# Performance work log

Measured on AMD Instinct MI355X. Metric: run time of the kernel, lower is better.

The kernel has to match this reference:

```python
import jax, jax.numpy as jnp
import numpy as np
from jax import lax

B, C, H, W, G = 16, 256, 96, 96, 16


def setup_inputs() -> dict:
    key = jax.random.key(0)
    ks = jax.random.split(key, 8)
    return {
        "x": jax.random.normal(ks[0], (B, C, H, W), jnp.float32),
        "in_w": jax.random.normal(ks[1], (C, C), jnp.float32) / np.sqrt(C).astype(np.float32),
        "gn1_w": jnp.ones((C,), jnp.float32),
        "gn1_b": jnp.zeros((C,), jnp.float32),
        "a_p": jnp.zeros((4, C), jnp.float32),   # torch init: zeros -> sigmoid = 0.5
        "b_p": jnp.ones((4, C), jnp.float32),
        "c_p": jnp.ones((4, C), jnp.float32),
        "d_p": jnp.ones((4, C), jnp.float32),
        "gate_w": jax.random.normal(ks[2], (C, C), jnp.float32) / np.sqrt(C).astype(np.float32),
        "gate_b": jnp.zeros((C,), jnp.float32),
        "dw_w": jax.random.normal(ks[3], (C, 1, 3, 3), jnp.float32) / 3.0,  # depthwise 3x3
        "pw_w": jax.random.normal(ks[4], (C, C), jnp.float32) / np.sqrt(C).astype(np.float32),
        "gn2_w": jnp.ones((C,), jnp.float32),
        "gn2_b": jnp.zeros((C,), jnp.float32),
    }


def group_norm(x, w, b, groups=G, eps=1e-5):
    Bn, Cn, Hn, Wn = x.shape
    xg = x.reshape(Bn, groups, Cn // groups, Hn, Wn)
    mu = xg.mean((2, 3, 4), keepdims=True)
    var = xg.var((2, 3, 4), keepdims=True)  # biased, matches torch GroupNorm
    xn = ((xg - mu) * lax.rsqrt(var + eps)).reshape(Bn, Cn, Hn, Wn)
    return xn * w[None, :, None, None] + b[None, :, None, None]


def scan_seq(seq, a, b, c, d):
    # seq: [N, C, L].  h_t = a*h_{t-1} + b*x_t ; y_t = c*h_t + d*x_t
    xs = jnp.moveaxis(seq, -1, 0)  # [L, N, C]
    def step(h, x_t):
        h = a * h + b * x_t
        return h, c * h + d * x_t
    h0 = jnp.zeros(xs.shape[1:], seq.dtype)
    _, ys = lax.scan(step, h0, xs)
    return jnp.moveaxis(ys, 0, -1)  # [N, C, L]


def scan_w(x, reverse, a, b, c, d):
    if reverse:
        x = x[:, :, :, ::-1]
    Bn, Cn, Hn, Wn = x.shape
    seq = x.transpose(0, 2, 1, 3).reshape(Bn * Hn, Cn, Wn)
    y = scan_seq(seq, a, b, c, d).reshape(Bn, Hn, Cn, Wn).transpose(0, 2, 1, 3)
    return y[:, :, :, ::-1] if reverse else y


def scan_h(x, reverse, a, b, c, d):
    if reverse:
        x = x[:, :, ::-1, :]
    Bn, Cn, Hn, Wn = x.shape
    seq = x.transpose(0, 3, 1, 2).reshape(Bn * Wn, Cn, Hn)
    y = scan_seq(seq, a, b, c, d).reshape(Bn, Wn, Cn, Hn).transpose(0, 2, 3, 1)
    return y[:, :, ::-1, :] if reverse else y


def reference(x, in_w, gn1_w, gn1_b, a_p, b_p, c_p, d_p, gate_w, gate_b, dw_w, pw_w, gn2_w, gn2_b):
    # in_proj: 1x1 conv (no bias) -> GroupNorm -> SiLU
    xp = jnp.einsum('oc,bchw->bohw', in_w, x)
    xp = jax.nn.silu(group_norm(xp, gn1_w, gn1_b))
    # 4-directional per-channel linear recurrences
    a = jax.nn.sigmoid(a_p)
    lr = scan_w(xp, False, a[0], b_p[0], c_p[0], d_p[0])
    rl = scan_w(xp, True,  a[1], b_p[1], c_p[1], d_p[1])
    tb = scan_h(xp, False, a[2], b_p[2], c_p[2], d_p[2])
    bt = scan_h(xp, True,  a[3], b_p[3], c_p[3], d_p[3])
    gate = jax.nn.sigmoid(jnp.einsum('oc,bchw->bohw', gate_w, xp) + gate_b[None, :, None, None])
    fused = 0.25 * (lr + rl + tb + bt) * gate
    # out_proj: depthwise 3x3 -> 1x1 conv -> GroupNorm -> SiLU
    dw = lax.conv_general_dilated(fused, dw_w, (1, 1), 'SAME',
                                  dimension_numbers=('NCHW', 'OIHW', 'NCHW'),
                                  feature_group_count=fused.shape[1])
    out = jnp.einsum('oc,bchw->bohw', pw_w, dw)
    return jax.nn.silu(group_norm(out, gn2_w, gn2_b))
```

## Files before the change

kernel.cpp:

```cpp
#include <hip/hip_runtime.h>
#include <hip/hip_bf16.h>

#define Bx 16
#define Cx 256
#define Hx 96
#define Wx 96
#define HWx 9216
#define NTOK 147456
#define Gx 16
#define GRPN 147456.0f

typedef unsigned short u16;
typedef unsigned int u32;
typedef __attribute__((ext_vector_type(8))) short short8;
typedef __attribute__((ext_vector_type(4))) float float4_;
typedef __attribute__((ext_vector_type(4))) unsigned short us4;
typedef __attribute__((ext_vector_type(8))) unsigned short us8;
typedef __attribute__((ext_vector_type(4))) unsigned int ui4;

__device__ __forceinline__ float b2f(u16 u){ u32 x = ((u32)u)<<16; float f; __builtin_memcpy(&f,&x,4); return f; }
__device__ __forceinline__ u16 f2b(float f){ u32 x; __builtin_memcpy(&x,&f,4); x += 0x7FFFu + ((x>>16)&1u); return (u16)(x>>16); }
__device__ __forceinline__ float sigm(float v){ return 1.0f/(1.0f+__expf(-v)); }

__global__ __launch_bounds__(256) void k_transpose(const float* __restrict__ X, u16* __restrict__ XT){
  __shared__ u16 tile[32][36];
  int blk = blockIdx.x;
  int ct  = blk & 7;
  int hwt = (blk >> 3) % 288;
  int b   = blk / 2304;
  int c0 = ct*32, hw0 = hwt*32;
  int t = threadIdx.x;
  int r  = t >> 3;
  int q4 = (t & 7) << 2;
  float4_ v = *(const float4_*)&X[((size_t)(b*Cx + c0 + r))*HWx + hw0 + q4];
  tile[r][q4+0]=f2b(v[0]); tile[r][q4+1]=f2b(v[1]); tile[r][q4+2]=f2b(v[2]); tile[r][q4+3]=f2b(v[3]);
  __syncthreads();
  us4 o = { tile[q4+0][r], tile[q4+1][r], tile[q4+2][r], tile[q4+3][r] };
  *(us4*)&XT[((size_t)(b*HWx + hw0 + r))*Cx + c0 + q4] = o;
}

#define BM 128
#define BN 64
#define LDA 40
#define LDB 264

template<int MODE>
__global__ __launch_bounds__(256) void k_gemm(const u16* __restrict__ A,
                                              const float* __restrict__ Wm,
                                              u16* __restrict__ Y,
                                              float* __restrict__ stats,
                                              const float* __restrict__ bias,
                                              u16* __restrict__ Sb)
{
  __shared__ u16 Ws[BN*LDB];
  __shared__ u16 As[BM*LDA];
  __shared__ float red[4][16][2];
  const int tid = threadIdx.x;
  int lin = blockIdx.x;
  int swz = (lin & 7) * 576 + (lin >> 3);
  const int n0 = (swz >> 2) * BM;
  const int o0 = (swz & 3) * BN;
  #pragma unroll
  for (int it=0; it<16; ++it){
    int cid = tid + it*256;
    int row = cid >> 6;
    int ko  = (cid & 63) << 2;
    float4_ w4 = *(const float4_*)&Wm[(size_t)(o0+row)*Cx + ko];
    us4 wb = { f2b(w4[0]), f2b(w4[1]), f2b(w4[2]), f2b(w4[3]) };
    *(us4*)&Ws[row*LDB + ko] = wb;
  }
  const int lane = tid & 63;
  const int wid  = tid >> 6;
  const int lm   = lane & 15;
  const int quad = lane >> 4;
  const int wn = wid & 1;
  const int wo = wid >> 1;
  float4_ acc[4][2];
  #pragma unroll
  for (int i=0;i<4;++i){ acc[i][0] = (float4_)0.0f; acc[i][1] = (float4_)0.0f; }
  for (int kk=0; kk<Cx; kk+=32){
    __syncthreads();
    #pragma unroll
    for (int it=0; it<2; ++it){
      int cid = tid + it*256;
      int r = cid >> 2;
      int ko = (cid & 3) << 3;
      *(ui4*)&As[r*LDA + ko] = *(const ui4*)&A[(size_t)(n0+r)*Cx + kk + ko];
    }
    __syncthreads();
    short8 af[4], bf[2];
    #pragma unroll
    for (int i=0;i<4;++i) af[i] = *(const short8*)&As[(wn*64 + i*16 + lm)*LDA + quad*8];
    #pragma unroll
    for (int j=0;j<2;++j) bf[j] = *(const short8*)&Ws[(wo*32 + j*16 + lm)*LDB + kk + quad*8];
    #pragma unroll
    for (int i=0;i<4;++i)
      #pragma unroll
      for (int j=0;j<2;++j)
        acc[i][j] = __builtin_amdgcn_mfma_f32_16x16x32_bf16(af[i], bf[j], acc[i][j], 0, 0, 0);
  }
  const int b = n0 / HWx;
  if (MODE == 1){
    #pragma unroll
    for (int i=0;i<4;++i){
      #pragma unroll
      for (int j=0;j<2;++j){
        int oc = o0 + wo*32 + j*16 + lm;
        float bb = bias[oc];
        #pragma unroll
        for (int r=0;r<4;++r){
          int row = n0 + wn*64 + i*16 + quad*4 + r;
          size_t idx = (size_t)row*Cx + oc;
          float g = sigm(acc[i][j][r] + bb);
          Y[idx] = f2b(0.25f * b2f(Sb[idx]) * g);
        }
      }
    }
  } else {
    float s0=0,s1=0,q0=0,q1=0;
    #pragma unroll
    for (int i=0;i<4;++i){
      #pragma unroll
      for (int j=0;j<2;++j){
        int oc = o0 + wo*32 + j*16 + lm;
        #pragma unroll
        for (int r=0;r<4;++r){
          int row = n0 + wn*64 + i*16 + quad*4 + r;
          float v = acc[i][j][r];
          Y[(size_t)row*Cx + oc] = f2b(v);
          if (j==0){ s0+=v; q0+=v*v; } else { s1+=v; q1+=v*v; }
        }
      }
    }
    s0 += __shfl_xor(s0,16); s0 += __shfl_xor(s0,32);
    q0 += __shfl_xor(q0,16); q0 += __shfl_xor(q0,32);
    s1 += __shfl_xor(s1,16); s1 += __shfl_xor(s1,32);
    q1 += __shfl_xor(q1,16); q1 += __shfl_xor(q1,32);
    if (tid < 128) ((float*)red)[tid] = 0.0f;
    __syncthreads();
    if (lane < 16){
      atomicAdd(&red[wo*2+0][lm][0], s0);
      atomicAdd(&red[wo*2+0][lm][1], q0);
      atomicAdd(&red[wo*2+1][lm][0], s1);
      atomicAdd(&red[wo*2+1][lm][1], q1);
    }
    __syncthreads();
    if (tid < 4){
      float ss=0, qq=0;
      #pragma unroll
      for (int k=0;k<16;++k){ ss += red[tid][k][0]; qq += red[tid][k][1]; }
      int g = (o0 >> 4) + tid;
      atomicAdd(&stats[(b*Gx + g)*2 + 0], ss);
      atomicAdd(&stats[(b*Gx + g)*2 + 1], qq);
    }
  }
}

__global__ void k_finalize(const float* __restrict__ st, float* __restrict__ mr){
  int i = threadIdx.x;
  float s = st[i*2+0], q = st[i*2+1];
  float mu  = s * (1.0f/GRPN);
  float var = q * (1.0f/GRPN) - mu*mu;
  mr[i*2+0] = mu;
  mr[i*2+1] = rsqrtf(var + 1e-5f);
}

__global__ __launch_bounds__(128) void k_scan_w(const u32* __restrict__ Y1, u32* __restrict__ Xp, u32* __restrict__ S,
    const float* __restrict__ ap, const float* __restrict__ bp, const float* __restrict__ cpr, const float* __restrict__ dp,
    const float* __restrict__ mr, const float* __restrict__ gwv, const float* __restrict__ gbv){
  int blk = blockIdx.x;
  int h = blk % Hx, b = blk / Hx;
  int t = threadIdx.x;
  int c = t*2;
  float A0a = sigm(ap[c]),   A0b = sigm(ap[c+1]);
  float B0a = bp[c],         B0b = bp[c+1];
  float C0a = cpr[c],        C0b = cpr[c+1];
  float D0a = dp[c],         D0b = dp[c+1];
  float A1a = sigm(ap[Cx+c]),A1b = sigm(ap[Cx+c+1]);
  float B1a = bp[Cx+c],      B1b = bp[Cx+c+1];
  float C1a = cpr[Cx+c],     C1b = cpr[Cx+c+1];
  float D1a = dp[Cx+c],      D1b = dp[Cx+c+1];
  int g = c >> 4;
  float mu = mr[(b*Gx+g)*2], rs = mr[(b*Gx+g)*2+1];
  float gwa = gwv[c], gba = gbv[c], gwb = gwv[c+1], gbb = gbv[c+1];
  const size_t base0 = ((size_t)(b*Hx + h)*Wx)*(Cx/2) + t;
  const u32* yp = Y1 + base0;
  u32* xp = Xp + base0;
  u32* sp = S  + base0;
  float hs0 = 0.0f, hs1 = 0.0f;
  #pragma unroll 4
  for (int w=0; w<Wx; ++w){
    u32 pk = *yp;
    float xna = (b2f((u16)(pk&0xffffu)) - mu)*rs*gwa + gba;
    float xnb = (b2f((u16)(pk>>16))     - mu)*rs*gwb + gbb;
    u16 va = f2b(xna * sigm(xna));
    u16 vb = f2b(xnb * sigm(xnb));
    *xp = (u32)va | ((u32)vb << 16);
    float x0 = b2f(va), x1 = b2f(vb);
    hs0 = A0a*hs0 + B0a*x0;
    hs1 = A0b*hs1 + B0b*x1;
    *sp = (u32)f2b(C0a*hs0 + D0a*x0) | ((u32)f2b(C0b*hs1 + D0b*x1) << 16);
    yp += 128; xp += 128; sp += 128;
  }
  asm volatile("" ::: "memory");
  hs0 = 0.0f; hs1 = 0.0f;
  #pragma unroll 4
  for (int w=0; w<Wx; ++w){
    xp -= 128; sp -= 128;
    u32 pk = *xp;
    float x0 = b2f((u16)(pk&0xffffu));
    float x1 = b2f((u16)(pk>>16));
    hs0 = A1a*hs0 + B1a*x0;
    hs1 = A1b*hs1 + B1b*x1;
    u32 sv = *sp;
    u16 oa = f2b(C1a*hs0 + D1a*x0 + b2f((u16)(sv&0xffffu)));
    u16 ob = f2b(C1b*hs1 + D1b*x1 + b2f((u16)(sv>>16)));
    *sp = (u32)oa | ((u32)ob << 16);
  }
}

__global__ __launch_bounds__(128) void k_scan_h(const u32* __restrict__ Xp, u32* __restrict__ S, u32* __restrict__ Av,
    const float* __restrict__ ap, const float* __restrict__ bp, const float* __restrict__ cpr, const float* __restrict__ dp){
  int blk = blockIdx.x;
  int w = blk % Wx, b = blk / Wx;
  int t = threadIdx.x;
  int c = t*2;
  float A2a = sigm(ap[2*Cx+c]), A2b = sigm(ap[2*Cx+c+1]);
  float B2a = bp[2*Cx+c],       B2b = bp[2*Cx+c+1];
  float C2a = cpr[2*Cx+c],      C2b = cpr[2*Cx+c+1];
  float D2a = dp[2*Cx+c],       D2b = dp[2*Cx+c+1];
  float A3a = sigm(ap[3*Cx+c]), A3b = sigm(ap[3*Cx+c+1]);
  float B3a = bp[3*Cx+c],       B3b = bp[3*Cx+c+1];
  float C3a = cpr[3*Cx+c],      C3b = cpr[3*Cx+c+1];
  float D3a = dp[3*Cx+c],       D3b = dp[3*Cx+c+1];
  const size_t base0 = ((size_t)(b*Hx)*Wx + w)*(Cx/2) + t;
  const u32* ip = Xp + base0;
  u32* av = Av + base0;
  u32* sp = S  + base0;
  float hs0 = 0.0f, hs1 = 0.0f;
  #pragma unroll 4
  for (int h=0; h<Hx; ++h){
    u32 pk = *ip;
    float x0 = b2f((u16)(pk&0xffffu));
    float x1 = b2f((u16)(pk>>16));
    hs0 = A2a*hs0 + B2a*x0;
    hs1 = A2b*hs1 + B2b*x1;
    *av = (u32)f2b(C2a*hs0 + D2a*x0) | ((u32)f2b(C2b*hs1 + D2b*x1) << 16);
    ip += Wx*128; av += Wx*128;
  }
  asm volatile("" ::: "memory");
  hs0 = 0.0f; hs1 = 0.0f;
  sp += (size_t)Hx*Wx*128;
  #pragma unroll 4
  for (int h=0; h<Hx; ++h){
    ip -= Wx*128; av -= Wx*128; sp -= Wx*128;
    u32 pk = *ip;
    float x0 = b2f((u16)(pk&0xffffu));
    float x1 = b2f((u16)(pk>>16));
    hs0 = A3a*hs0 + B3a*x0;
    hs1 = A3b*hs1 + B3b*x1;
    u32 akk = *av;
    u32 sv  = *sp;
    u16 oa = f2b(C3a*hs0 + D3a*x0 + b2f((u16)(akk&0xffffu)) + b2f((u16)(sv&0xffffu)));
    u16 ob = f2b(C3b*hs1 + D3b*x1 + b2f((u16)(akk>>16))     + b2f((u16)(sv>>16)));
    *sp = (u32)oa | ((u32)ob << 16);
  }
}

__global__ __launch_bounds__(256) void k_dwconv(const u16* __restrict__ F, const float* __restrict__ dwW, u16* __restrict__ O){
  __shared__ float wl[2304];
  int t = threadIdx.x;
  #pragma unroll
  for (int i=0;i<9;++i) wl[t + i*256] = dwW[t + i*256];
  __syncthreads();
  int blk = blockIdx.x;
  int w16 = blk % (Wx/16);
  int h   = (blk/(Wx/16)) % Hx;
  int b   = blk / ((Wx/16)*Hx);
  int cq = (t & 63) << 2;
  int w0 = (w16 << 4) + ((t >> 6) << 2);
  float wt[36];
  #pragma unroll
  for (int j=0;j<9;++j) *(float4_*)&wt[4*j] = *(const float4_*)&wl[cq*9 + 4*j];
  float acc[4][4];
  #pragma unroll
  for (int ow=0;ow<4;++ow){ acc[ow][0]=0.0f; acc[ow][1]=0.0f; acc[ow][2]=0.0f; acc[ow][3]=0.0f; }
  const u16* Fb = F + ((size_t)(b*Hx)*Wx)*Cx + cq;
  #pragma unroll
  for (int ky=0; ky<3; ++ky){
    int hh = h + ky - 1;
    if (hh < 0 || hh >= Hx) continue;
    #pragma unroll
    for (int j=0; j<6; ++j){
      int ww = w0 + j - 1;
      if (ww < 0 || ww >= Wx) continue;
      us4 v = *(const us4*)&Fb[((size_t)hh*Wx + ww)*Cx];
      float f0=b2f(v[0]), f1=b2f(v[1]), f2=b2f(v[2]), f3=b2f(v[3]);
      #pragma unroll
      for (int ow = (j-2<0?0:j-2); ow <= (j<3?j:3); ++ow){
        int kidx = ky*3 + (j - ow);
        acc[ow][0] += f0 * wt[0*9 + kidx];
        acc[ow][1] += f1 * wt[1*9 + kidx];
        acc[ow][2] += f2 * wt[2*9 + kidx];
        acc[ow][3] += f3 * wt[3*9 + kidx];
      }
    }
  }
  #pragma unroll
  for (int ow=0; ow<4; ++ow){
    us4 o = { f2b(acc[ow][0]), f2b(acc[ow][1]), f2b(acc[ow][2]), f2b(acc[ow][3]) };
    *(us4*)&O[((size_t)((b*Hx+h)*Wx) + w0 + ow)*Cx + cq] = o;
  }
}

__global__ __launch_bounds__(256) void k_norm_tr(const u16* __restrict__ Y3, float* __restrict__ Out,
    const float* __restrict__ mr, const float* __restrict__ gw, const float* __restrict__ gb){
  __shared__ float tile[32][36];
  int blk = blockIdx.x;
  int ct  = blk & 7;
  int hwt = (blk >> 3) % 288;
  int b   = blk / 2304;
  int c0 = ct*32, hw0 = hwt*32;
  int t = threadIdx.x;
  int r  = t >> 3;
  int q4 = (t & 7) << 2;
  us4 v = *(const us4*)&Y3[((size_t)(b*HWx + hw0 + r))*Cx + c0 + q4];
  int g = (c0 + q4) >> 4;
  float mu = mr[(b*Gx+g)*2], rs = mr[(b*Gx+g)*2+1];
  #pragma unroll
  for (int i=0;i<4;++i){
    float xn = (b2f(v[i]) - mu)*rs*gw[c0+q4+i] + gb[c0+q4+i];
    tile[r][q4+i] = xn * sigm(xn);
  }
  __syncthreads();
  float4_ o = { tile[q4+0][r], tile[q4+1][r], tile[q4+2][r], tile[q4+3][r] };
  *(float4_*)&Out[((size_t)(b*Cx + c0 + r))*HWx + hw0 + q4] = o;
}

extern "C" void kernel_launch(void* const* d_in, const int* in_sizes, int n_in,
                              void* d_out, int out_size, void* d_ws, size_t ws_size,
                              hipStream_t stream){
  (void)in_sizes; (void)n_in; (void)out_size; (void)ws_size;
  const float* x    = (const float*)d_in[0];
  const float* in_w = (const float*)d_in[1];
  const float* gn1w = (const float*)d_in[2];
  const float* gn1b = (const float*)d_in[3];
  const float* ap   = (const float*)d_in[4];
  const float* bp   = (const float*)d_in[5];
  const float* cp   = (const float*)d_in[6];
  const float* dp   = (const float*)d_in[7];
  const float* gw   = (const float*)d_in[8];
  const float* gb   = (const float*)d_in[9];
  const float* dww  = (const float*)d_in[10];
  const float* pww  = (const float*)d_in[11];
  const float* gn2w = (const float*)d_in[12];
  const float* gn2b = (const float*)d_in[13];
  float* out = (float*)d_out;
  char* ws = (char*)d_ws;
  const size_t NB = (size_t)NTOK * Cx * 2;
  u16* xT = (u16*)(ws);
  u16* y1 = (u16*)(ws + NB);
  u16* xp = (u16*)(ws + 2*NB);
  u16* S  = (u16*)(ws + 3*NB);
  float* stats1 = (float*)(ws + 4*NB);
  float* stats2 = stats1 + 512;
  float* mr1    = stats1 + 1024;
  float* mr2    = stats1 + 1536;

  hipMemsetAsync(stats1, 0, 1024*sizeof(float), stream);

  k_transpose<<<36864, 256, 0, stream>>>(x, xT);
  k_gemm<0><<<4608, 256, 0, stream>>>(xT, in_w, y1, stats1, nullptr, nullptr);
  k_finalize<<<1, 256, 0, stream>>>(stats1, mr1);
  k_scan_w<<<Bx*Hx, 128, 0, stream>>>((const u32*)y1, (u32*)xp, (u32*)S, ap, bp, cp, dp, mr1, gn1w, gn1b);
  k_scan_h<<<Bx*Wx, 128, 0, stream>>>((const u32*)xp, (u32*)S, (u32*)xT, ap, bp, cp, dp);
  k_gemm<1><<<4608, 256, 0, stream>>>(xp, gw, S, nullptr, gb, S);
  k_dwconv<<<Bx*Hx*(Wx/16), 256, 0, stream>>>(S, dww, xT);
  k_gemm<0><<<4608, 256, 0, stream>>>(xT, pww, y1, stats2, nullptr, nullptr);
  k_finalize<<<1, 256, 0, stream>>>(stats2, mr2);
  k_norm_tr<<<36864, 256, 0, stream>>>(y1, out, mr2, gn2w, gn2b);
}
```

Baseline: 756.2 us.

## Run horizontal and vertical scans concurrently in one kernel launch

Merges the W-direction and H-direction scan kernels into a single launch whose blocks split between row and column scans. Column blocks now recompute the GroupNorm+SiLU activation from the raw GEMM output instead of waiting on the row pass, and write into a separate buffer. The gate GEMM epilogue sums the two partial buffers. This removes a serial dependency and a launch, and the small grids (1536 blocks each) can fill the GPU together. The cost is extra recomputation of the normalisation in the column pass and one more buffer read in the gate epilogue.

Measured after the change: 830.4 us. +9.8%, slower.

```diff
diff --git a/kernel.cpp b/kernel.cpp
--- a/kernel.cpp
+++ b/kernel.cpp
@@ -50,7 +50,8 @@
                                               u16* __restrict__ Y,
                                               float* __restrict__ stats,
                                               const float* __restrict__ bias,
-                                              u16* __restrict__ Sb)
+                                              const u16* __restrict__ Sb,
+                                              const u16* __restrict__ Sb2)
 {
   __shared__ u16 Ws[BN*LDB];
   __shared__ u16 As[BM*LDA];
@@ -112,7 +113,8 @@
           int row = n0 + wn*64 + i*16 + quad*4 + r;
           size_t idx = (size_t)row*Cx + oc;
           float g = sigm(acc[i][j][r] + bb);
-          Y[idx] = f2b(0.25f * b2f(Sb[idx]) * g);
+          float s = b2f(Sb[idx]) + b2f(Sb2[idx]);
+          Y[idx] = f2b(0.25f * s * g);
         }
       }
     }
@@ -165,105 +167,106 @@
   mr[i*2+1] = rsqrtf(var + 1e-5f);
 }
 
-__global__ __launch_bounds__(128) void k_scan_w(const u32* __restrict__ Y1, u32* __restrict__ Xp, u32* __restrict__ S,
+__global__ __launch_bounds__(128) void k_scan2(const u32* __restrict__ Y1, u32* __restrict__ Xp,
+    u32* __restrict__ Sw, u32* __restrict__ Sh,
     const float* __restrict__ ap, const float* __restrict__ bp, const float* __restrict__ cpr, const float* __restrict__ dp,
     const float* __restrict__ mr, const float* __restrict__ gwv, const float* __restrict__ gbv){
   int blk = blockIdx.x;
-  int h = blk % Hx, b = blk / Hx;
   int t = threadIdx.x;
   int c = t*2;
-  float A0a = sigm(ap[c]),   A0b = sigm(ap[c+1]);
-  float B0a = bp[c],         B0b = bp[c+1];
-  float C0a = cpr[c],        C0b = cpr[c+1];
-  float D0a = dp[c],         D0b = dp[c+1];
-  float A1a = sigm(ap[Cx+c]),A1b = sigm(ap[Cx+c+1]);
-  float B1a = bp[Cx+c],      B1b = bp[Cx+c+1];
-  float C1a = cpr[Cx+c],     C1b = cpr[Cx+c+1];
-  float D1a = dp[Cx+c],      D1b = dp[Cx+c+1];
   int g = c >> 4;
-  float mu = mr[(b*Gx+g)*2], rs = mr[(b*Gx+g)*2+1];
-  float gwa = gwv[c], gba = gbv[c], gwb = gwv[c+1], gbb = gbv[c+1];
-  const size_t base0 = ((size_t)(b*Hx + h)*Wx)*(Cx/2) + t;
-  const u32* yp = Y1 + base0;
-  u32* xp = Xp + base0;
-  u32* sp = S  + base0;
-  float hs0 = 0.0f, hs1 = 0.0f;
-  #pragma unroll 4
-  for (int w=0; w<Wx; ++w){
-    u32 pk = *yp;
-    float xna = (b2f((u16)(pk&0xffffu)) - mu)*rs*gwa + gba;
-    float xnb = (b2f((u16)(pk>>16))     - mu)*rs*gwb + gbb;
-    u16 va = f2b(xna * sigm(xna));
-    u16 vb = f2b(xnb * sigm(xnb));
-    *xp = (u32)va | ((u32)vb << 16);
-    float x0 = b2f(va), x1 = b2f(vb);
-    hs0 = A0a*hs0 + B0a*x0;
-    hs1 = A0b*hs1 + B0b*x1;
-    *sp = (u32)f2b(C0a*hs0 + D0a*x0) | ((u32)f2b(C0b*hs1 + D0b*x1) << 16);
-    yp += 128; xp += 128; sp += 128;
-  }
-  asm volatile("" ::: "memory");
-  hs0 = 0.0f; hs1 = 0.0f;
-  #pragma unroll 4
-  for (int w=0; w<Wx; ++w){
-    xp -= 128; sp -= 128;
-    u32 pk = *xp;
-    float x0 = b2f((u16)(pk&0xffffu));
-    float x1 = b2f((u16)(pk>>16));
-    hs0 = A1a*hs0 + B1a*x0;
-    hs1 = A1b*hs1 + B1b*x1;
-    u32 sv = *sp;
-    u16 oa = f2b(C1a*hs0 + D1a*x0 + b2f((u16)(sv&0xffffu)));
-    u16 ob = f2b(C1b*hs1 + D1b*x1 + b2f((u16)(sv>>16)));
-    *sp = (u32)oa | ((u32)ob << 16);
-  }
-}
-
-__global__ __launch_bounds__(128) void k_scan_h(const u32* __restrict__ Xp, u32* __restrict__ S, u32* __restrict__ Av,
-    const float* __restrict__ ap, const float* __restrict__ bp, const float* __restrict__ cpr, const float* __restrict__ dp){
-  int blk = blockIdx.x;
-  int w = blk % Wx, b = blk / Wx;
-  int t = threadIdx.x;
-  int c = t*2;
-  float A2a = sigm(ap[2*Cx+c]), A2b = sigm(ap[2*Cx+c+1]);
-  float B2a = bp[2*Cx+c],       B2b = bp[2*Cx+c+1];
-  float C2a = cpr[2*Cx+c],      C2b = cpr[2*Cx+c+1];
-  float D2a = dp[2*Cx+c],       D2b = dp[2*Cx+c+1];
-  float A3a = sigm(ap[3*Cx+c]), A3b = sigm(ap[3*Cx+c+1]);
-  float B3a = bp[3*Cx+c],       B3b = bp[3*Cx+c+1];
-  float C3a = cpr[3*Cx+c],      C3b = cpr[3*Cx+c+1];
-  float D3a = dp[3*Cx+c],       D3b = dp[3*Cx+c+1];
-  const size_t base0 = ((size_t)(b*Hx)*Wx + w)*(Cx/2) + t;
-  const u32* ip = Xp + base0;
-  u32* av = Av + base0;
-  u32* sp = S  + base0;
-  float hs0 = 0.0f, hs1 = 0.0f;
-  #pragma unroll 4
-  for (int h=0; h<Hx; ++h){
-    u32 pk = *ip;
-    float x0 = b2f((u16)(pk&0xffffu));
-    float x1 = b2f((u16)(pk>>16));
-    hs0 = A2a*hs0 + B2a*x0;
-    hs1 = A2b*hs1 + B2b*x1;
-    *av = (u32)f2b(C2a*hs0 + D2a*x0) | ((u32)f2b(C2b*hs1 + D2b*x1) << 16);
-    ip += Wx*128; av += Wx*128;
-  }
-  asm volatile("" ::: "memory");
-  hs0 = 0.0f; hs1 = 0.0f;
-  sp += (size_t)Hx*Wx*128;
-  #pragma unroll 4
-  for (int h=0; h<Hx; ++h){
-    ip -= Wx*128; av -= Wx*128; sp -= Wx*128;
-    u32 pk = *ip;
-    float x0 = b2f((u16)(pk&0xffffu));
-    float x1 = b2f((u16)(pk>>16));
-    hs0 = A3a*hs0 + B3a*x0;
-    hs1 = A3b*hs1 + B3b*x1;
-    u32 akk = *av;
-    u32 sv  = *sp;
-    u16 oa = f2b(C3a*hs0 + D3a*x0 + b2f((u16)(akk&0xffffu)) + b2f((u16)(sv&0xffffu)));
-    u16 ob = f2b(C3b*hs1 + D3b*x1 + b2f((u16)(akk>>16))     + b2f((u16)(sv>>16)));
-    *sp = (u32)oa | ((u32)ob << 16);
+  if (blk < Bx*Hx){
+    int h = blk % Hx, b = blk / Hx;
+    float A0a = sigm(ap[c]),   A0b = sigm(ap[c+1]);
+    float B0a = bp[c],         B0b = bp[c+1];
+    float C0a = cpr[c],        C0b = cpr[c+1];
+    float D0a = dp[c],         D0b = dp[c+1];
+    float A1a = sigm(ap[Cx+c]),A1b = sigm(ap[Cx+c+1]);
+    float B1a = bp[Cx+c],      B1b = bp[Cx+c+1];
+    float C1a = cpr[Cx+c],     C1b = cpr[Cx+c+1];
+    float D1a = dp[Cx+c],      D1b = dp[Cx+c+1];
+    float mu = mr[(b*Gx+g)*2], rs = mr[(b*Gx+g)*2+1];
+    float gwa = gwv[c], gba = gbv[c], gwb = gwv[c+1], gbb = gbv[c+1];
+    const size_t base0 = ((size_t)(b*Hx + h)*Wx)*(Cx/2) + t;
+    const u32* yp = Y1 + base0;
+    u32* xp = Xp + base0;
+    u32* sp = Sw + base0;
+    float hs0 = 0.0f, hs1 = 0.0f;
+    #pragma unroll 4
+    for (int w=0; w<Wx; ++w){
+      u32 pk = *yp;
+      float xna = (b2f((u16)(pk&0xffffu)) - mu)*rs*gwa + gba;
+      float xnb = (b2f((u16)(pk>>16))     - mu)*rs*gwb + gbb;
+      u16 va = f2b(xna * sigm(xna));
+      u16 vb = f2b(xnb * sigm(xnb));
+      *xp = (u32)va | ((u32)vb << 16);
+      float x0 = b2f(va), x1 = b2f(vb);
+      hs0 = A0a*hs0 + B0a*x0;
+      hs1 = A0b*hs1 + B0b*x1;
+      *sp = (u32)f2b(C0a*hs0 + D0a*x0) | ((u32)f2b(C0b*hs1 + D0b*x1) << 16);
+      yp += 128; xp += 128; sp += 128;
+    }
+    asm volatile("" ::: "memory");
+    hs0 = 0.0f; hs1 = 0.0f;
+    #pragma unroll 4
+    for (int w=0; w<Wx; ++w){
+      xp -= 128; sp -= 128;
+      u32 pk = *xp;
+      float x0 = b2f((u16)(pk&0xffffu));
+      float x1 = b2f((u16)(pk>>16));
+      hs0 = A1a*hs0 + B1a*x0;
+      hs1 = A1b*hs1 + B1b*x1;
+      u32 sv = *sp;
+      u16 oa = f2b(C1a*hs0 + D1a*x0 + b2f((u16)(sv&0xffffu)));
+      u16 ob = f2b(C1b*hs1 + D1b*x1 + b2f((u16)(sv>>16)));
+      *sp = (u32)oa | ((u32)ob << 16);
+    }
+  } else {
+    int col = blk - Bx*Hx;
+    int w = col % Wx, b = col / Wx;
+    float A2a = sigm(ap[2*Cx+c]), A2b = sigm(ap[2*Cx+c+1]);
+    float B2a = bp[2*Cx+c],       B2b = bp[2*Cx+c+1];
+    float C2a = cpr[2*Cx+c],      C2b = cpr[2*Cx+c+1];
+    float D2a = dp[2*Cx+c],       D2b = dp[2*Cx+c+1];
+    float A3a = sigm(ap[3*Cx+c]), A3b = sigm(ap[3*Cx+c+1]);
+    float B3a = bp[3*Cx+c],       B3b = bp[3*Cx+c+1];
+    float C3a = cpr[3*Cx+c],      C3b = cpr[3*Cx+c+1];
+    float D3a = dp[3*Cx+c],       D3b = dp[3*Cx+c+1];
+    float mu = mr[(b*Gx+g)*2], rs = mr[(b*Gx+g)*2+1];
+    float gwa = gwv[c], gba = gbv[c], gwb = gwv[c+1], gbb = gbv[c+1];
+    const size_t base0 = ((size_t)(b*Hx)*Wx + w)*(Cx/2) + t;
+    const u32* yp = Y1 + base0;
+    u32* sp = Sh + base0;
+    float hs0 = 0.0f, hs1 = 0.0f;
+    #pragma unroll 4
+    for (int h=0; h<Hx; ++h){
+      u32 pk = *yp;
+      float xna = (b2f((u16)(pk&0xffffu)) - mu)*rs*gwa + gba;
+      float xnb = (b2f((u16)(pk>>16))     - mu)*rs*gwb + gbb;
+      float x0 = b2f(f2b(xna * sigm(xna)));
+      float x1 = b2f(f2b(xnb * sigm(xnb)));
+      hs0 = A2a*hs0 + B2a*x0;
+      hs1 = A2b*hs1 + B2b*x1;
+      *sp = (u32)f2b(C2a*hs0 + D2a*x0) | ((u32)f2b(C2b*hs1 + D2b*x1) << 16);
+      yp += Wx*128; sp += Wx*128;
+    }
+    asm volatile("" ::: "memory");
+    hs0 = 0.0f; hs1 = 0.0f;
+    #pragma unroll 4
+    for (int h=0; h<Hx; ++h){
+      yp -= Wx*128; sp -= Wx*128;
+      u32 pk = *yp;
+      float xna = (b2f((u16)(pk&0xffffu)) - mu)*rs*gwa + gba;
+      float xnb = (b2f((u16)(pk>>16))     - mu)*rs*gwb + gbb;
+      float x0 = b2f(f2b(xna * sigm(xna)));
+      float x1 = b2f(f2b(xnb * sigm(xnb)));
+      hs0 = A3a*hs0 + B3a*x0;
+      hs1 = A3b*hs1 + B3b*x1;
+      u32 sv = *sp;
+      u16 oa = f2b(C3a*hs0 + D3a*x0 + b2f((u16)(sv&0xffffu)));
+      u16 ob = f2b(C3b*hs1 + D3b*x1 + b2f((u16)(sv>>16)));
+      *sp = (u32)oa | ((u32)ob << 16);
+    }
   }
 }
 
@@ -370,13 +373,13 @@
   hipMemsetAsync(stats1, 0, 1024*sizeof(float), stream);
 
   k_transpose<<<36864, 256, 0, stream>>>(x, xT);
-  k_gemm<0><<<4608, 256, 0, stream>>>(xT, in_w, y1, stats1, nullptr, nullptr);
+  k_gemm<0><<<4608, 256, 0, stream>>>(xT, in_w, y1, stats1, nullptr, nullptr, nullptr);
   k_finalize<<<1, 256, 0, stream>>>(stats1, mr1);
-  k_scan_w<<<Bx*Hx, 128, 0, stream>>>((const u32*)y1, (u32*)xp, (u32*)S, ap, bp, cp, dp, mr1, gn1w, gn1b);
-  k_scan_h<<<Bx*Wx, 128, 0, stream>>>((const u32*)xp, (u32*)S, (u32*)xT, ap, bp, cp, dp);
-  k_gemm<1><<<4608, 256, 0, stream>>>(xp, gw, S, nullptr, gb, S);
-  k_dwconv<<<Bx*Hx*(Wx/16), 256, 0, stream>>>(S, dww, xT);
-  k_gemm<0><<<4608, 256, 0, stream>>>(xT, pww, y1, stats2, nullptr, nullptr);
+  k_scan2<<<Bx*Hx + Bx*Wx, 128, 0, stream>>>((const u32*)y1, (u32*)xp, (u32*)S, (u32*)xT,
+                                             ap, bp, cp, dp, mr1, gn1w, gn1b);
+  k_gemm<1><<<4608, 256, 0, stream>>>(xp, gw, S, nullptr, gb, S, xT);
+  k_dwconv<<<Bx*Hx*(Wx/16), 256, 0, stream>>>(S, dww, xp);
+  k_gemm<0><<<4608, 256, 0, stream>>>(xp, pww, y1, stats2, nullptr, nullptr, nullptr);
   k_finalize<<<1, 256, 0, stream>>>(stats2, mr2);
   k_norm_tr<<<36864, 256, 0, stream>>>(y1, out, mr2, gn2w, gn2b);
 }
```
